# Performance work log

Hardware: AMD Instinct MI355X
Metric: run time of the kernel (lower is better)

## Reference

```python
import jax, jax.numpy as jnp
import numpy as np


def setup_inputs() -> dict:
    key = jax.random.key(0)
    k1, k2 = jax.random.split(key)
    N, C, H, W = 4, 128, 160, 320
    left = jax.random.normal(k1, (N, C, H, W), dtype=jnp.float32)
    right = jax.random.normal(k2, (N, C, H, W), dtype=jnp.float32)
    return {"left": left, "right": right, "max_disparity": 48}


def reference(left, right, max_disparity):
    # left, right: (N, C, H, W) -> volume: (N, D, H, W)
    # volume[n, d, h, w] = sum_c left[n, c, h, w] * right[n, c, h, w - d]  (0 if w < d)
    n, c, h, w = left.shape
    slices = []
    for d in range(max_disparity):  # fixed structural constant, unrolled at trace time
        # channel dot-product of overlapping strips, shape (N, H, W - d)
        corr = jnp.einsum('nchw,nchw->nhw', left[:, :, :, d:], right[:, :, :, :w - d])
        # left-pad the first d columns with zeros to restore width W
        slices.append(jnp.pad(corr, ((0, 0), (0, 0), (d, 0))))
    return jnp.stack(slices, axis=1)  # (N, D, H, W)
```

## Files before the change

### kernel.cpp

```cpp
#include <hip/hip_runtime.h>


#define NN 4
#define CC 128
#define HH 160
#define WW 320
#define DD 48
#define HWs (HH * WW)
#define WB 80
#define RROWS 128
#define RPITCH 132
#define RTASKS 2048
#define NTHREADS 320

typedef _Float16 h2 __attribute__((ext_vector_type(2)));
typedef _Float16 f16x8 __attribute__((ext_vector_type(8)));
typedef float f32x4 __attribute__((ext_vector_type(4)));
typedef __fp16 h2raw __attribute__((ext_vector_type(2)));

__device__ __forceinline__ h2 pack2(float a, float b) {
  union { h2raw r; h2 h; } u;
  u.r = __builtin_amdgcn_cvt_pkrtz(a, b);
  return u.h;
}

__global__ __launch_bounds__(NTHREADS, 5)
void corr_kernel(const float* __restrict__ L, const float* __restrict__ R,
                 float* __restrict__ out) {
  __shared__ __align__(16) h2 Rh[64][RPITCH];

  const int tid = threadIdx.x;
  const int wt  = tid >> 6;
  const int ln  = tid & 63;
  const int i16 = ln & 15;
  const int g   = ln >> 4;

  const int bid = blockIdx.x;
  const int wsplit = bid & 3;
  const int row_nh = bid >> 2;
  const int n = row_nh / HH;
  const int h = row_nh - n * HH;
  const int wb = wsplit * WB;

  const size_t base = (size_t)n * CC * HWs + (size_t)h * WW;
  const float* Rbase = R + base;
  const float* Lbase = L + base + wb + 16 * wt + i16;

  union F4 { float4 f; float a[4]; };
  F4 ra[7], rc[7];
#pragma unroll
  for (int it = 0; it < 7; ++it) {
    int t = tid + it * NTHREADS;
    ra[it].f = make_float4(0.f, 0.f, 0.f, 0.f);
    rc[it].f = make_float4(0.f, 0.f, 0.f, 0.f);
    if (t < RTASKS) {
      int c2 = t >> 5, v = t & 31;
      int col = wb - 48 + 4 * v;
      if (col >= 0) {
        const float* p = Rbase + (size_t)(2 * c2) * HWs + col;
        ra[it].f = *(const float4*)p;
        rc[it].f = *(const float4*)(p + HWs);
      }
    }
  }

  float lv[32];
#pragma unroll
  for (int ks = 0; ks < 4; ++ks)
#pragma unroll
    for (int e = 0; e < 8; ++e)
      lv[ks * 8 + e] = Lbase[(size_t)(32 * ks + 8 * g + e) * HWs];

  union V4 { float4 f; h2 h[4]; };
#pragma unroll
  for (int it = 0; it < 7; ++it) {
    int t = tid + it * NTHREADS;
    if (t < RTASKS) {
      int c2 = t >> 5, v = t & 31;
      V4 u;
#pragma unroll
      for (int i = 0; i < 4; ++i) u.h[i] = pack2(ra[it].a[i], rc[it].a[i]);
      *(float4*)&Rh[c2][4 * v] = u.f;
    }
  }

  union AU { f16x8 v; h2 h[4]; };
  AU A[4];
#pragma unroll
  for (int ks = 0; ks < 4; ++ks)
#pragma unroll
    for (int j = 0; j < 4; ++j)
      A[ks].h[j] = pack2(lv[ks * 8 + 2 * j], lv[ks * 8 + 2 * j + 1]);

  __syncthreads();

  f32x4 acc[4] = {};
#pragma unroll
  for (int q = 0; q < 4; ++q) {
    const int j = 16 * (wt + q) + i16;
    union BU { f16x8 v; h2 h[4]; } B;
#pragma unroll
    for (int ks = 0; ks < 4; ++ks) {
      const int r0 = 16 * ks + 4 * g;
#pragma unroll
      for (int r = 0; r < 4; ++r) B.h[r] = Rh[r0 + r][j];
      acc[q] = __builtin_amdgcn_mfma_f32_16x16x32_f16(A[ks].v, B.v, acc[q], 0, 0, 0);
    }
  }

  __syncthreads();

  float* Ep = ((float*)&Rh[0][0]) + wt * (DD * 20);
#pragma unroll
  for (int q = 0; q < 4; ++q)
#pragma unroll
    for (int r = 0; r < 4; ++r) {
      int d = 48 - 16 * q + 4 * g + r - i16;
      if (d >= 0 && d < DD) Ep[d * 20 + 4 * g + r] = acc[q][r];
    }

  const int l4 = ln & 3;
  const int dr = ln >> 2;
  float* outp = out + (size_t)n * DD * HWs + (size_t)h * WW + wb + 16 * wt + 4 * l4;
#pragma unroll
  for (int rr = 0; rr < 3; ++rr) {
    int d = 16 * rr + dr;
    float4 val = *(const float4*)&Ep[d * 20 + 4 * l4];
    *(float4*)&outp[(size_t)d * HWs] = val;
  }
}

extern "C" void kernel_launch(void* const* d_in, const int* in_sizes, int n_in,
                              void* d_out, int out_size, void* d_ws, size_t ws_size,
                              hipStream_t stream) {
  const float* L = (const float*)d_in[0];
  const float* R = (const float*)d_in[1];
  float* out = (float*)d_out;
  corr_kernel<<<dim3(4 * NN * HH), dim3(NTHREADS), 0, stream>>>(L, R, out);
}
```

Before: 244.7 us.

## Process full rows per block with a circular LDS ring and prefetch

Each block now handles a whole image row, looping over four 80-column chunks instead of launching one block per chunk. The right-image strip is kept in a circular shared-memory ring so the 48-column disparity halo is not reloaded. The next chunk's left/right data is loaded into registers while MFMAs run on the current one. This cuts redundant global reads and hides load latency, at the cost of a quarter as many blocks, more registers and LDS, and lower occupancy.

```diff
diff --git a/kernel.cpp b/kernel.cpp
--- a/kernel.cpp
+++ b/kernel.cpp
@@ -7,11 +7,9 @@
 #define WW 320
 #define DD 48
 #define HWs (HH * WW)
-#define WB 80
-#define RROWS 128
-#define RPITCH 132
-#define RTASKS 2048
-#define NTHREADS 320
+#define RS 208
+#define RP 212
+#define NTH 320
 
 typedef _Float16 h2 __attribute__((ext_vector_type(2)));
 typedef _Float16 f16x8 __attribute__((ext_vector_type(8)));
@@ -24,10 +22,11 @@
   return u.h;
 }
 
-__global__ __launch_bounds__(NTHREADS, 5)
+__global__ __launch_bounds__(NTH, 3)
 void corr_kernel(const float* __restrict__ L, const float* __restrict__ R,
                  float* __restrict__ out) {
-  __shared__ __align__(16) h2 Rh[64][RPITCH];
+  __shared__ __align__(16) h2 Rh[64][RP];
+  __shared__ __align__(16) float Ep[5][DD * 20];
 
   const int tid = threadIdx.x;
   const int wt  = tid >> 6;
@@ -36,97 +35,131 @@
   const int g   = ln >> 4;
 
   const int bid = blockIdx.x;
-  const int wsplit = bid & 3;
-  const int row_nh = bid >> 2;
-  const int n = row_nh / HH;
-  const int h = row_nh - n * HH;
-  const int wb = wsplit * WB;
-
+  const int n = bid / HH;
+  const int h = bid - n * HH;
   const size_t base = (size_t)n * CC * HWs + (size_t)h * WW;
-  const float* Rbase = R + base;
-  const float* Lbase = L + base + wb + 16 * wt + i16;
+  const float* Rb = R + base;
+  const float* Lb = L + base + 16 * wt + i16;
 
   union F4 { float4 f; float a[4]; };
-  F4 ra[7], rc[7];
+  union V4 { float4 f; h2 h[4]; };
+  union AU { f16x8 v; h2 h[4]; };
+  union BU { f16x8 v; h2 h[4]; };
+
+  float lv[2][32];
+  {
+    F4 ra[7], rc[7];
 #pragma unroll
-  for (int it = 0; it < 7; ++it) {
-    int t = tid + it * NTHREADS;
-    ra[it].f = make_float4(0.f, 0.f, 0.f, 0.f);
-    rc[it].f = make_float4(0.f, 0.f, 0.f, 0.f);
-    if (t < RTASKS) {
-      int c2 = t >> 5, v = t & 31;
-      int col = wb - 48 + 4 * v;
-      if (col >= 0) {
-        const float* p = Rbase + (size_t)(2 * c2) * HWs + col;
+    for (int it = 0; it < 7; ++it) {
+      int t = tid + it * NTH;
+      ra[it].f = make_float4(0.f, 0.f, 0.f, 0.f);
+      rc[it].f = make_float4(0.f, 0.f, 0.f, 0.f);
+      if (t < 2048) {
+        int c2 = t >> 5, v = t & 31;
+        int col = 4 * v - 48;
+        if (col >= 0) {
+          const float* p = Rb + (size_t)(2 * c2) * HWs + col;
+          ra[it].f = *(const float4*)p;
+          rc[it].f = *(const float4*)(p + HWs);
+        }
+      }
+    }
+#pragma unroll
+    for (int ks = 0; ks < 4; ++ks)
+#pragma unroll
+      for (int e = 0; e < 8; ++e)
+        lv[0][ks * 8 + e] = Lb[(size_t)(32 * ks + 8 * g + e) * HWs];
+#pragma unroll
+    for (int it = 0; it < 7; ++it) {
+      int t = tid + it * NTH;
+      if (t < 2048) {
+        int c2 = t >> 5, v = t & 31;
+        V4 u;
+#pragma unroll
+        for (int i = 0; i < 4; ++i) u.h[i] = pack2(ra[it].a[i], rc[it].a[i]);
+        *(float4*)&Rh[c2][4 * v] = u.f;
+      }
+    }
+  }
+  __syncthreads();
+
+#pragma unroll
+  for (int k = 0; k < 4; ++k) {
+    const int cur = k & 1, nxt = cur ^ 1;
+
+    AU A[4];
+#pragma unroll
+    for (int ks = 0; ks < 4; ++ks)
+#pragma unroll
+      for (int j = 0; j < 4; ++j)
+        A[ks].h[j] = pack2(lv[cur][ks * 8 + 2 * j], lv[cur][ks * 8 + 2 * j + 1]);
+
+    F4 ra[4], rc[4];
+    if (k < 3) {
+      const int j0 = 80 * (k + 1);
+#pragma unroll
+      for (int it = 0; it < 4; ++it) {
+        int t = tid + it * NTH;
+        int c2 = t / 20, v = t - 20 * c2;
+        const float* p = Rb + (size_t)(2 * c2) * HWs + (j0 + 4 * v);
         ra[it].f = *(const float4*)p;
         rc[it].f = *(const float4*)(p + HWs);
       }
-    }
-  }
-
-  float lv[32];
+      const float* Lp = Lb + 80 * (k + 1);
 #pragma unroll
-  for (int ks = 0; ks < 4; ++ks)
+      for (int ks = 0; ks < 4; ++ks)
 #pragma unroll
-    for (int e = 0; e < 8; ++e)
-      lv[ks * 8 + e] = Lbase[(size_t)(32 * ks + 8 * g + e) * HWs];
-
-  union V4 { float4 f; h2 h[4]; };
-#pragma unroll
-  for (int it = 0; it < 7; ++it) {
-    int t = tid + it * NTHREADS;
-    if (t < RTASKS) {
-      int c2 = t >> 5, v = t & 31;
-      V4 u;
-#pragma unroll
-      for (int i = 0; i < 4; ++i) u.h[i] = pack2(ra[it].a[i], rc[it].a[i]);
-      *(float4*)&Rh[c2][4 * v] = u.f;
-    }
-  }
-
-  union AU { f16x8 v; h2 h[4]; };
-  AU A[4];
-#pragma unroll
-  for (int ks = 0; ks < 4; ++ks)
-#pragma unroll
-    for (int j = 0; j < 4; ++j)
-      A[ks].h[j] = pack2(lv[ks * 8 + 2 * j], lv[ks * 8 + 2 * j + 1]);
-
-  __syncthreads();
-
-  f32x4 acc[4] = {};
-#pragma unroll
-  for (int q = 0; q < 4; ++q) {
-    const int j = 16 * (wt + q) + i16;
-    union BU { f16x8 v; h2 h[4]; } B;
-#pragma unroll
-    for (int ks = 0; ks < 4; ++ks) {
-      const int r0 = 16 * ks + 4 * g;
-#pragma unroll
-      for (int r = 0; r < 4; ++r) B.h[r] = Rh[r0 + r][j];
-      acc[q] = __builtin_amdgcn_mfma_f32_16x16x32_f16(A[ks].v, B.v, acc[q], 0, 0, 0);
-    }
-  }
-
-  __syncthreads();
-
-  float* Ep = ((float*)&Rh[0][0]) + wt * (DD * 20);
-#pragma unroll
-  for (int q = 0; q < 4; ++q)
-#pragma unroll
-    for (int r = 0; r < 4; ++r) {
-      int d = 48 - 16 * q + 4 * g + r - i16;
-      if (d >= 0 && d < DD) Ep[d * 20 + 4 * g + r] = acc[q][r];
+        for (int e = 0; e < 8; ++e)
+          lv[nxt][ks * 8 + e] = Lp[(size_t)(32 * ks + 8 * g + e) * HWs];
     }
 
-  const int l4 = ln & 3;
-  const int dr = ln >> 2;
-  float* outp = out + (size_t)n * DD * HWs + (size_t)h * WW + wb + 16 * wt + 4 * l4;
+    f32x4 acc[4];
 #pragma unroll
-  for (int rr = 0; rr < 3; ++rr) {
-    int d = 16 * rr + dr;
-    float4 val = *(const float4*)&Ep[d * 20 + 4 * l4];
-    *(float4*)&outp[(size_t)d * HWs] = val;
+    for (int q = 0; q < 4; ++q) {
+      acc[q] = (f32x4){0.f, 0.f, 0.f, 0.f};
+      int s = 80 * k + 16 * (wt + q) + i16;
+      if (s >= RS) s -= RS;
+      BU B;
+#pragma unroll
+      for (int ks = 0; ks < 4; ++ks) {
+        const int r0 = 16 * ks + 4 * g;
+#pragma unroll
+        for (int r = 0; r < 4; ++r) B.h[r] = Rh[r0 + r][s];
+        acc[q] = __builtin_amdgcn_mfma_f32_16x16x32_f16(A[ks].v, B.v, acc[q], 0, 0, 0);
+      }
+    }
+
+    if (k < 3) {
+#pragma unroll
+      for (int it = 0; it < 4; ++it) {
+        int t = tid + it * NTH;
+        int c2 = t / 20, v = t - 20 * c2;
+        int s = 80 * (k + 1) + 48 + 4 * v;
+        if (s >= RS) s -= RS;
+        V4 u;
+#pragma unroll
+        for (int i = 0; i < 4; ++i) u.h[i] = pack2(ra[it].a[i], rc[it].a[i]);
+        *(float4*)&Rh[c2][s] = u.f;
+      }
+    }
+    __syncthreads();
+
+    float* ep = Ep[wt];
+#pragma unroll
+    for (int q = 0; q < 4; ++q)
+#pragma unroll
+      for (int r = 0; r < 4; ++r) {
+        int d = 48 - 16 * q + 4 * g + r - i16;
+        if (d >= 0 && d < DD) ep[d * 20 + 4 * g + r] = acc[q][r];
+      }
+    const int l4 = ln & 3;
+    const int dr = ln >> 2;
+    float* op = out + (size_t)n * DD * HWs + (size_t)h * WW + 80 * k + 16 * wt + 4 * l4;
+#pragma unroll
+    for (int rr = 0; rr < 3; ++rr) {
+      int d = 16 * rr + dr;
+      *(float4*)&op[(size_t)d * HWs] = *(const float4*)&ep[d * 20 + 4 * l4];
+    }
   }
 }
 
@@ -136,5 +169,5 @@
   const float* L = (const float*)d_in[0];
   const float* R = (const float*)d_in[1];
   float* out = (float*)d_out;
-  corr_kernel<<<dim3(4 * NN * HH), dim3(NTHREADS), 0, stream>>>(L, R, out);
+  corr_kernel<<<dim3(NN * HH), dim3(NTH), 0, stream>>>(L, R, out);
 }
```

Result: no change. 244.4 us (-0.1%).
